# Kernel tuning notes

Measured on AMD Instinct MI355X. Metric: run time of the kernel, lower is better.

The kernel has to match this reference:

```python
import jax, jax.numpy as jnp
import numpy as np

B, C, H, W = 8, 192, 64, 64
RED = 8
CR = C // RED  # 24


def prelu(x, a):
    # a is a single shared slope (PyTorch nn.PReLU() default num_parameters=1)
    return jnp.where(x >= 0, x, a * x)


def conv1x1(x, w, b):
    # x: [B,C,H,W], w: [O,C], b: [O] -> [B,O,H,W]
    return jnp.einsum('bchw,oc->bohw', x, w) + b[None, :, None, None]


def setup_inputs() -> dict:
    key = jax.random.key(0)
    ks = jax.random.split(key, 7)
    scale1 = 1.0 / np.sqrt(C)
    return {
        'x': jax.random.normal(ks[0], (B, C, H, W), dtype=jnp.float32),
        'w1': jax.random.uniform(ks[1], (CR, C), jnp.float32, -scale1, scale1),
        'b1': jnp.zeros((CR,), jnp.float32),
        'a1': jnp.full((1,), 0.25, jnp.float32),
        'w2': jax.random.uniform(ks[2], (CR, C), jnp.float32, -scale1, scale1),
        'b2': jnp.zeros((CR,), jnp.float32),
        'a2': jnp.full((1,), 0.25, jnp.float32),
        'wa': jax.random.uniform(ks[3], (C, C), jnp.float32, -scale1, scale1),
        'ba': jnp.zeros((C,), jnp.float32),
        'aa': jnp.full((1,), 0.25, jnp.float32),
    }


def reference(x, w1, b1, a1, w2, b2, a2, wa, ba, aa):
    b, c, h, w = x.shape
    hw = h * w
    q = prelu(conv1x1(x, w1, b1), a1)          # [B,Cr,H,W]
    k = prelu(conv1x1(x, w2, b2), a2)          # [B,Cr,H,W]
    v = prelu(conv1x1(x, wa, ba), aa)          # [B,C,H,W]
    q = q.reshape(b, -1, hw).transpose(0, 2, 1)   # [B,HW,Cr]
    k = k.reshape(b, -1, hw)                      # [B,Cr,HW]
    score = jax.nn.softmax(jnp.einsum('bnc,bcm->bnm', q, k), axis=2)  # [B,HW,HW]
    v = v.reshape(b, c, hw).transpose(0, 2, 1)    # [B,HW,C]
    out = jnp.einsum('bnm,bmc->bnc', score, v)    # [B,HW,C]
    return out.transpose(0, 2, 1).reshape(b, c, h, w)
```

## Files before the change

kernel.cpp:

```cpp
#include <hip/hip_runtime.h>
#include <hip/hip_fp16.h>

#define HW 4096
#define NC 192
#define NB 8
#define DQK 32
#define LOG2E 1.4426950408889634f
#define THRL 11.541560327f

typedef _Float16 f16x8 __attribute__((ext_vector_type(8)));
typedef float f32x4 __attribute__((ext_vector_type(4)));
typedef unsigned int u32x4 __attribute__((ext_vector_type(4)));

#define BAR() do { asm volatile("s_waitcnt lgkmcnt(0)" ::: "memory"); \
                   __builtin_amdgcn_s_barrier();                      \
                   asm volatile("" ::: "memory"); } while (0)

static __device__ __forceinline__ unsigned int pkrtz(float a, float b) {
  auto h = __builtin_amdgcn_cvt_pkrtz(a, b);
  return __builtin_bit_cast(unsigned int, h);
}
static __device__ __forceinline__ unsigned short f2h_bits(float f) {
  _Float16 h = (_Float16)f;
  union { _Float16 h; unsigned short u; } cv; cv.h = h; return cv.u;
}

__global__ void wtrans_kernel(
    const float* __restrict__ w1, const float* __restrict__ b1, const float* __restrict__ a1,
    const float* __restrict__ w2, const float* __restrict__ b2, const float* __restrict__ a2,
    const float* __restrict__ wa, const float* __restrict__ ba, const float* __restrict__ aa,
    float* __restrict__ wt)
{
  const int c = blockIdx.x;
  const int o = threadIdx.x;
  if (o >= 240) return;
  float v;
  if (c < 192) {
    if (o < 24)      v = w1[o * 192 + c];
    else if (o < 48) v = w2[(o - 24) * 192 + c];
    else             v = wa[(o - 48) * 192 + c];
  } else if (c == 192) {
    v = (o < 24) ? b1[o] : (o < 48) ? b2[o - 24] : ba[o - 48];
  } else {
    v = (o < 24) ? a1[0] : (o < 48) ? a2[0] : aa[0];
  }
  wt[c * 240 + o] = v;
}

__global__ __launch_bounds__(256) void proj_kernel(
    const float* __restrict__ x, const float* __restrict__ wt,
    unsigned short* __restrict__ Qn, unsigned short* __restrict__ Kn,
    unsigned short* __restrict__ Vt)
{
  const int g   = blockIdx.y;
  const int tid = threadIdx.x;
  const int bp  = (blockIdx.x * 256 + tid) * 2;
  const int b   = bp >> 12;
  const int pos = bp & (HW - 1);

  const float* xb = x + (size_t)b * NC * HW + pos;
  float acc0[16], acc1[16];
  #pragma unroll
  for (int o = 0; o < 16; ++o) { acc0[o] = 0.f; acc1[o] = 0.f; }

  #pragma unroll 4
  for (int c = 0; c < 192; ++c) {
    float2 xv = *reinterpret_cast<const float2*>(xb + (size_t)c * HW);
    const float* wr = wt + c * 240 + g * 16;
    #pragma unroll
    for (int o = 0; o < 16; ++o) {
      float w = wr[o];
      acc0[o] = fmaf(w, xv.x, acc0[o]);
      acc1[o] = fmaf(w, xv.y, acc1[o]);
    }
  }

  const float* brow = wt + 192 * 240 + g * 16;
  const float* srow = wt + 193 * 240 + g * 16;
  unsigned short h0[16], h1[16];
  #pragma unroll
  for (int o = 0; o < 16; ++o) {
    float bias = brow[o], sm1 = srow[o] - 1.f;
    float v0 = acc0[o] + bias; v0 += fminf(v0, 0.f) * sm1;
    float v1 = acc1[o] + bias; v1 += fminf(v1, 0.f) * sm1;
    if (g * 16 + o < 24) { v0 *= LOG2E; v1 *= LOG2E; }
    h0[o] = f2h_bits(v0);
    h1[o] = f2h_bits(v1);
  }

  if (g >= 3) {
    const int vch0 = g * 16 - 48;
    unsigned int* vp = reinterpret_cast<unsigned int*>(
        Vt + ((size_t)b * NC + vch0) * HW + pos);
    #pragma unroll
    for (int o = 0; o < 16; ++o)
      vp[o * (HW / 2)] = (unsigned int)h0[o] | ((unsigned int)h1[o] << 16);
  } else {
    u32x4 lo0, hi0, lo1, hi1;
    #pragma unroll
    for (int j = 0; j < 4; ++j) {
      lo0[j] = (unsigned int)h0[2 * j] | ((unsigned int)h0[2 * j + 1] << 16);
      hi0[j] = (unsigned int)h0[8 + 2 * j] | ((unsigned int)h0[9 + 2 * j] << 16);
      lo1[j] = (unsigned int)h1[2 * j] | ((unsigned int)h1[2 * j + 1] << 16);
      hi1[j] = (unsigned int)h1[8 + 2 * j] | ((unsigned int)h1[9 + 2 * j] << 16);
    }
    const size_t bpos = (size_t)b * HW + pos;
    if (g == 0) {
      u32x4* q0 = reinterpret_cast<u32x4*>(Qn + bpos * DQK);
      q0[0] = lo0; q0[1] = hi0;
      u32x4* q1 = reinterpret_cast<u32x4*>(Qn + (bpos + 1) * DQK);
      q1[0] = lo1; q1[1] = hi1;
    } else if (g == 1) {
      *reinterpret_cast<u32x4*>(Qn + bpos * DQK + 16) = lo0;
      *reinterpret_cast<u32x4*>(Kn + bpos * DQK) = hi0;
      *reinterpret_cast<u32x4*>(Qn + (bpos + 1) * DQK + 16) = lo1;
      *reinterpret_cast<u32x4*>(Kn + (bpos + 1) * DQK) = hi1;
    } else {
      u32x4* k0 = reinterpret_cast<u32x4*>(Kn + bpos * DQK + 8);
      k0[0] = lo0; k0[1] = hi0;
      u32x4* k1 = reinterpret_cast<u32x4*>(Kn + (bpos + 1) * DQK + 8);
      k1[0] = lo1; k1[1] = hi1;
    }
  }
}

__global__ __launch_bounds__(512, 4) void flash_kernel(
    const unsigned short* __restrict__ Qn, const unsigned short* __restrict__ Kn,
    const unsigned short* __restrict__ Vt, float* __restrict__ out)
{
  const int b    = blockIdx.y;
  const int q0   = blockIdx.x * 64;
  const int tid  = threadIdx.x;
  const int w    = tid >> 6;
  const int half = w >> 2;
  const int wi   = w & 3;
  const int lane = tid & 63;
  const int lq   = lane & 15;
  const int lk   = lane >> 4;

  __shared__ u32x4 Pex[2][2][4][2][64];
  __shared__ float alphaL[2][2][4][16];
  __shared__ float mlL[2][2][64];

  const int mbase = half * (HW / 2);
  const int sigb  = 8 * (lq >> 2) + (lq & 3);

  f16x8 qfrag = *reinterpret_cast<const f16x8*>(
      Qn + ((size_t)b * HW + q0 + 16 * wi + lq) * DQK + 8 * lk);

  float m = -1e30f;
  f32x4 O[12], lacc;
  #pragma unroll
  for (int i = 0; i < 12; ++i) O[i] = (f32x4){0.f, 0.f, 0.f, 0.f};
  lacc = (f32x4){0.f, 0.f, 0.f, 0.f};

  const unsigned short* Kb = Kn + (size_t)b * HW * DQK + (size_t)sigb * DQK + 8 * lk;
  const unsigned short* Vw = Vt + (size_t)b * NC * HW + (size_t)(wi * 48 + lq) * HW + 8 * lk;

  f16x8 vones;
  #pragma unroll
  for (int i = 0; i < 8; ++i) vones[i] = (_Float16)1.0f;

  f16x8 Kf[4];

  auto qk_softmax = [&](int par) {
    f32x4 s[4];
    #pragma unroll
    for (int t = 0; t < 4; ++t)
      s[t] = __builtin_amdgcn_mfma_f32_16x16x32_f16(Kf[t], qfrag,
              (f32x4){0.f, 0.f, 0.f, 0.f}, 0, 0, 0);
    float pmax = s[0][0];
    #pragma unroll
    for (int t = 0; t < 4; ++t)
      #pragma unroll
      for (int r = 0; r < 4; ++r) pmax = fmaxf(pmax, s[t][r]);
    float alpha = 1.f;
    if (__any(pmax > m + THRL)) {
      pmax = fmaxf(pmax, __shfl_xor(pmax, 16));
      pmax = fmaxf(pmax, __shfl_xor(pmax, 32));
      float mn = fmaxf(m, pmax);
      alpha = exp2f(m - mn);
      m = mn;
    }
    float pv[4][4];
    #pragma unroll
    for (int t = 0; t < 4; ++t)
      #pragma unroll
      for (int r = 0; r < 4; ++r) pv[t][r] = exp2f(s[t][r] - m);
    u32x4 pa0, pa1;
    pa0[0] = pkrtz(pv[0][0], pv[0][1]); pa0[1] = pkrtz(pv[0][2], pv[0][3]);
    pa0[2] = pkrtz(pv[2][0], pv[2][1]); pa0[3] = pkrtz(pv[2][2], pv[2][3]);
    pa1[0] = pkrtz(pv[1][0], pv[1][1]); pa1[1] = pkrtz(pv[1][2], pv[1][3]);
    pa1[2] = pkrtz(pv[3][0], pv[3][1]); pa1[3] = pkrtz(pv[3][2], pv[3][3]);
    Pex[par][half][wi][0][lane] = pa0;
    Pex[par][half][wi][1][lane] = pa1;
    if (lane < 16) alphaL[par][half][wi][lane] = alpha;
  };

  #pragma unroll
  for (int t = 0; t < 4; ++t)
    Kf[t] = *reinterpret_cast<const f16x8*>(
        Kb + (size_t)(mbase + 32 * (t & 1) + 4 * (t >> 1)) * DQK);
  qk_softmax(0);
  BAR();

  const int NIT = HW / 2 / 64;
  for (int it = 0; it < NIT; ++it) {
    const int prt = it & 1;
    const bool notlast = (it + 1 < NIT);
    const int m0 = mbase + it * 64;
    const int mnext = m0 + 64;
    if (notlast) {
      #pragma unroll
      for (int t = 0; t < 4; ++t)
        Kf[t] = *reinterpret_cast<const f16x8*>(
            Kb + (size_t)(mnext + 32 * (t & 1) + 4 * (t >> 1)) * DQK);
    }
    #pragma unroll
    for (int tr = 0; tr < 4; ++tr) {
      f32x4 al = *reinterpret_cast<const f32x4*>(&alphaL[prt][half][tr][4 * lk]);
      int diff = (al[0] != 1.f) | (al[1] != 1.f) | (al[2] != 1.f) | (al[3] != 1.f);
      if (__any(diff)) {
        #pragma unroll
        for (int tc = 0; tc < 3; ++tc) {
          O[tr * 3 + tc][0] *= al[0]; O[tr * 3 + tc][1] *= al[1];
          O[tr * 3 + tc][2] *= al[2]; O[tr * 3 + tc][3] *= al[3];
        }
        if (tr == wi) {
          lacc[0] *= al[0]; lacc[1] *= al[1]; lacc[2] *= al[2]; lacc[3] *= al[3];
        }
      }
    }
    {
      f16x8 paf[4];
      #pragma unroll
      for (int tr = 0; tr < 4; ++tr)
        paf[tr] = __builtin_bit_cast(f16x8, Pex[prt][half][tr][0][lane]);
      f16x8 pw = __builtin_bit_cast(f16x8, Pex[prt][half][wi][0][lane]);
      lacc = __builtin_amdgcn_mfma_f32_16x16x32_f16(pw, vones, lacc, 0, 0, 0);
      #pragma unroll
      for (int tc = 0; tc < 3; ++tc) {
        f16x8 vb = *reinterpret_cast<const f16x8*>(
            Vw + (size_t)tc * 16 * HW + m0);
        #pragma unroll
        for (int tr = 0; tr < 4; ++tr)
          O[tr * 3 + tc] = __builtin_amdgcn_mfma_f32_16x16x32_f16(
              paf[tr], vb, O[tr * 3 + tc], 0, 0, 0);
      }
    }
    if (notlast) qk_softmax(prt ^ 1);
    {
      f16x8 paf[4];
      #pragma unroll
      for (int tr = 0; tr < 4; ++tr)
        paf[tr] = __builtin_bit_cast(f16x8, Pex[prt][half][tr][1][lane]);
      f16x8 pw = __builtin_bit_cast(f16x8, Pex[prt][half][wi][1][lane]);
      lacc = __builtin_amdgcn_mfma_f32_16x16x32_f16(pw, vones, lacc, 0, 0, 0);
      #pragma unroll
      for (int tc = 0; tc < 3; ++tc) {
        f16x8 vb = *reinterpret_cast<const f16x8*>(
            Vw + (size_t)tc * 16 * HW + m0 + 32);
        #pragma unroll
        for (int tr = 0; tr < 4; ++tr)
          O[tr * 3 + tc] = __builtin_amdgcn_mfma_f32_16x16x32_f16(
              paf[tr], vb, O[tr * 3 + tc], 0, 0, 0);
      }
    }
    BAR();
  }

  if (lane < 16) mlL[half][0][16 * wi + lane] = m;
  if (lq == 0) {
    #pragma unroll
    for (int r = 0; r < 4; ++r) mlL[half][1][16 * wi + 4 * lk + r] = lacc[r];
  }
  f32x4* Ost = reinterpret_cast<f32x4*>(&Pex[0][0][0][0][0]);
  if (half == 1) {
    #pragma unroll
    for (int i = 0; i < 8; ++i) Ost[(wi * 8 + i) * 64 + lane] = O[i];
  }
  BAR();
  f32x4 f0v[4], f1v[4];
  if (half == 0) {
    #pragma unroll
    for (int tr = 0; tr < 4; ++tr) {
      f32x4 m0v = *reinterpret_cast<const f32x4*>(&mlL[0][0][16 * tr + 4 * lk]);
      f32x4 l0v = *reinterpret_cast<const f32x4*>(&mlL[0][1][16 * tr + 4 * lk]);
      f32x4 m1v = *reinterpret_cast<const f32x4*>(&mlL[1][0][16 * tr + 4 * lk]);
      f32x4 l1v = *reinterpret_cast<const f32x4*>(&mlL[1][1][16 * tr + 4 * lk]);
      #pragma unroll
      for (int r = 0; r < 4; ++r) {
        float M  = fmaxf(m0v[r], m1v[r]);
        float s0 = exp2f(m0v[r] - M), s1 = exp2f(m1v[r] - M);
        float L  = s0 * l0v[r] + s1 * l1v[r];
        f0v[tr][r] = s0 / L; f1v[tr][r] = s1 / L;
      }
    }
    #pragma unroll
    for (int i = 0; i < 8; ++i) {
      const int tr = i / 3, tc = i - tr * 3;
      f32x4 o1 = Ost[(wi * 8 + i) * 64 + lane];
      f32x4 o;
      #pragma unroll
      for (int r = 0; r < 4; ++r) o[r] = O[i][r] * f0v[tr][r] + o1[r] * f1v[tr][r];
      *reinterpret_cast<f32x4*>(
          out + ((size_t)b * NC + wi * 48 + tc * 16 + lq) * HW + q0 + 16 * tr + 4 * lk) = o;
    }
  }
  BAR();
  if (half == 1) {
    #pragma unroll
    for (int i = 0; i < 4; ++i) Ost[(wi * 4 + i) * 64 + lane] = O[8 + i];
  }
  BAR();
  if (half == 0) {
    #pragma unroll
    for (int i = 8; i < 12; ++i) {
      const int tr = i / 3, tc = i - tr * 3;
      f32x4 o1 = Ost[(wi * 4 + (i - 8)) * 64 + lane];
      f32x4 o;
      #pragma unroll
      for (int r = 0; r < 4; ++r) o[r] = O[i][r] * f0v[tr][r] + o1[r] * f1v[tr][r];
      *reinterpret_cast<f32x4*>(
          out + ((size_t)b * NC + wi * 48 + tc * 16 + lq) * HW + q0 + 16 * tr + 4 * lk) = o;
    }
  }
}

extern "C" void kernel_launch(void* const* d_in, const int* in_sizes, int n_in,
                              void* d_out, int out_size, void* d_ws, size_t ws_size,
                              hipStream_t stream) {
  const float* x  = (const float*)d_in[0];
  const float* w1 = (const float*)d_in[1];
  const float* b1 = (const float*)d_in[2];
  const float* a1 = (const float*)d_in[3];
  const float* w2 = (const float*)d_in[4];
  const float* b2 = (const float*)d_in[5];
  const float* a2 = (const float*)d_in[6];
  const float* wa = (const float*)d_in[7];
  const float* ba = (const float*)d_in[8];
  const float* aa = (const float*)d_in[9];
  float* out = (float*)d_out;

  unsigned short* Qn = (unsigned short*)d_ws;
  unsigned short* Kn = Qn + (size_t)NB * HW * DQK;
  unsigned short* Vt = Kn + (size_t)NB * HW * DQK;
  float* wt = out + (out_size - 49152);

  (void)hipMemsetAsync(Qn, 0, (size_t)NB * HW * DQK * 2 * sizeof(unsigned short), stream);

  wtrans_kernel<<<dim3(194), 256, 0, stream>>>(w1, b1, a1, w2, b2, a2, wa, ba, aa, wt);

  dim3 pgrid(HW * NB / 512, 15);
  proj_kernel<<<pgrid, 256, 0, stream>>>(x, wt, Qn, Kn, Vt);

  dim3 fgrid(HW / 64, NB);
  flash_kernel<<<fgrid, 512, 0, stream>>>(Qn, Kn, Vt, out);
}
```

Before: 184.0 us.

## Restructure projection to 48 channels per thread and hoist V loads with MFMA priority

```diff
diff --git a/kernel.cpp b/kernel.cpp
--- a/kernel.cpp
+++ b/kernel.cpp
@@ -53,74 +53,57 @@
     unsigned short* __restrict__ Vt)
 {
   const int g   = blockIdx.y;
-  const int tid = threadIdx.x;
-  const int bp  = (blockIdx.x * 256 + tid) * 2;
+  const int bp  = blockIdx.x * 256 + threadIdx.x;
   const int b   = bp >> 12;
   const int pos = bp & (HW - 1);
+  const int ob  = 48 * g;
 
   const float* xb = x + (size_t)b * NC * HW + pos;
-  float acc0[16], acc1[16];
-  #pragma unroll
-  for (int o = 0; o < 16; ++o) { acc0[o] = 0.f; acc1[o] = 0.f; }
-
-  #pragma unroll 4
+  float acc[48];
+  #pragma unroll
+  for (int o = 0; o < 48; ++o) acc[o] = 0.f;
+
+  #pragma unroll 2
   for (int c = 0; c < 192; ++c) {
-    float2 xv = *reinterpret_cast<const float2*>(xb + (size_t)c * HW);
-    const float* wr = wt + c * 240 + g * 16;
-    #pragma unroll
-    for (int o = 0; o < 16; ++o) {
-      float w = wr[o];
-      acc0[o] = fmaf(w, xv.x, acc0[o]);
-      acc1[o] = fmaf(w, xv.y, acc1[o]);
-    }
-  }
-
-  const float* brow = wt + 192 * 240 + g * 16;
-  const float* srow = wt + 193 * 240 + g * 16;
-  unsigned short h0[16], h1[16];
-  #pragma unroll
-  for (int o = 0; o < 16; ++o) {
+    float xv = xb[(size_t)c * HW];
+    const float* wr = wt + c * 240 + ob;
+    #pragma unroll
+    for (int o = 0; o < 48; ++o) acc[o] = fmaf(wr[o], xv, acc[o]);
+  }
+
+  const float* brow = wt + 192 * 240 + ob;
+  const float* srow = wt + 193 * 240 + ob;
+  unsigned short h[48];
+  #pragma unroll
+  for (int o = 0; o < 48; ++o) {
     float bias = brow[o], sm1 = srow[o] - 1.f;
-    float v0 = acc0[o] + bias; v0 += fminf(v0, 0.f) * sm1;
-    float v1 = acc1[o] + bias; v1 += fminf(v1, 0.f) * sm1;
-    if (g * 16 + o < 24) { v0 *= LOG2E; v1 *= LOG2E; }
-    h0[o] = f2h_bits(v0);
-    h1[o] = f2h_bits(v1);
-  }
-
-  if (g >= 3) {
-    const int vch0 = g * 16 - 48;
-    unsigned int* vp = reinterpret_cast<unsigned int*>(
-        Vt + ((size_t)b * NC + vch0) * HW + pos);
-    #pragma unroll
-    for (int o = 0; o < 16; ++o)
-      vp[o * (HW / 2)] = (unsigned int)h0[o] | ((unsigned int)h1[o] << 16);
+    float v = acc[o] + bias; v += fminf(v, 0.f) * sm1;
+    if (g == 0 && o < 24) v *= LOG2E;
+    h[o] = f2h_bits(v);
+  }
+
+  if (g == 0) {
+    const size_t bpos = (size_t)bp;
+    u32x4 u;
+    #pragma unroll
+    for (int j = 0; j < 3; ++j) {
+      #pragma unroll
+      for (int i = 0; i < 4; ++i)
+        u[i] = (unsigned int)h[8 * j + 2 * i] | ((unsigned int)h[8 * j + 2 * i + 1] << 16);
+      *reinterpret_cast<u32x4*>(Qn + bpos * DQK + 8 * j) = u;
+    }
+    #pragma unroll
+    for (int j = 0; j < 3; ++j) {
+      #pragma unroll
+      for (int i = 0; i < 4; ++i)
+        u[i] = (unsigned int)h[24 + 8 * j + 2 * i] | ((unsigned int)h[25 + 8 * j + 2 * i] << 16);
+      *reinterpret_cast<u32x4*>(Kn + bpos * DQK + 8 * j) = u;
+    }
   } else {
-    u32x4 lo0, hi0, lo1, hi1;
-    #pragma unroll
-    for (int j = 0; j < 4; ++j) {
-      lo0[j] = (unsigned int)h0[2 * j] | ((unsigned int)h0[2 * j + 1] << 16);
-      hi0[j] = (unsigned int)h0[8 + 2 * j] | ((unsigned int)h0[9 + 2 * j] << 16);
-      lo1[j] = (unsigned int)h1[2 * j] | ((unsigned int)h1[2 * j + 1] << 16);
-      hi1[j] = (unsigned int)h1[8 + 2 * j] | ((unsigned int)h1[9 + 2 * j] << 16);
-    }
-    const size_t bpos = (size_t)b * HW + pos;
-    if (g == 0) {
-      u32x4* q0 = reinterpret_cast<u32x4*>(Qn + bpos * DQK);
-      q0[0] = lo0; q0[1] = hi0;
-      u32x4* q1 = reinterpret_cast<u32x4*>(Qn + (bpos + 1) * DQK);
-      q1[0] = lo1; q1[1] = hi1;
-    } else if (g == 1) {
-      *reinterpret_cast<u32x4*>(Qn + bpos * DQK + 16) = lo0;
-      *reinterpret_cast<u32x4*>(Kn + bpos * DQK) = hi0;
-      *reinterpret_cast<u32x4*>(Qn + (bpos + 1) * DQK + 16) = lo1;
-      *reinterpret_cast<u32x4*>(Kn + (bpos + 1) * DQK) = hi1;
-    } else {
-      u32x4* k0 = reinterpret_cast<u32x4*>(Kn + bpos * DQK + 8);
-      k0[0] = lo0; k0[1] = hi0;
-      u32x4* k1 = reinterpret_cast<u32x4*>(Kn + (bpos + 1) * DQK + 8);
-      k1[0] = lo1; k1[1] = hi1;
-    }
+    const int vch0 = 48 * (g - 1);
+    #pragma unroll
+    for (int o = 0; o < 48; ++o)
+      Vt[((size_t)b * NC + vch0 + o) * HW + pos] = h[o];
   }
 }
 
@@ -128,8 +111,8 @@
     const unsigned short* __restrict__ Qn, const unsigned short* __restrict__ Kn,
     const unsigned short* __restrict__ Vt, float* __restrict__ out)
 {
-  const int b    = blockIdx.y;
-  const int q0   = blockIdx.x * 64;
+  const int b    = blockIdx.x & 7;
+  const int q0   = (blockIdx.x >> 3) * 64;
   const int tid  = threadIdx.x;
   const int w    = tid >> 6;
   const int half = w >> 2;
@@ -210,6 +193,10 @@
     const bool notlast = (it + 1 < NIT);
     const int m0 = mbase + it * 64;
     const int mnext = m0 + 64;
+    f16x8 vb0[3];
+    #pragma unroll
+    for (int tc = 0; tc < 3; ++tc)
+      vb0[tc] = *reinterpret_cast<const f16x8*>(Vw + (size_t)tc * 16 * HW + m0);
     if (notlast) {
       #pragma unroll
       for (int t = 0; t < 4; ++t)
@@ -237,17 +224,20 @@
       for (int tr = 0; tr < 4; ++tr)
         paf[tr] = __builtin_bit_cast(f16x8, Pex[prt][half][tr][0][lane]);
       f16x8 pw = __builtin_bit_cast(f16x8, Pex[prt][half][wi][0][lane]);
+      __builtin_amdgcn_s_setprio(1);
       lacc = __builtin_amdgcn_mfma_f32_16x16x32_f16(pw, vones, lacc, 0, 0, 0);
       #pragma unroll
-      for (int tc = 0; tc < 3; ++tc) {
-        f16x8 vb = *reinterpret_cast<const f16x8*>(
-            Vw + (size_t)tc * 16 * HW + m0);
+      for (int tc = 0; tc < 3; ++tc)
         #pragma unroll
         for (int tr = 0; tr < 4; ++tr)
           O[tr * 3 + tc] = __builtin_amdgcn_mfma_f32_16x16x32_f16(
-              paf[tr], vb, O[tr * 3 + tc], 0, 0, 0);
-      }
-    }
+              paf[tr], vb0[tc], O[tr * 3 + tc], 0, 0, 0);
+      __builtin_amdgcn_s_setprio(0);
+    }
+    f16x8 vb1[3];
+    #pragma unroll
+    for (int tc = 0; tc < 3; ++tc)
+      vb1[tc] = *reinterpret_cast<const f16x8*>(Vw + (size_t)tc * 16 * HW + m0 + 32);
     if (notlast) qk_softmax(prt ^ 1);
     {
       f16x8 paf[4];
@@ -255,16 +245,15 @@
       for (int tr = 0; tr < 4; ++tr)
         paf[tr] = __builtin_bit_cast(f16x8, Pex[prt][half][tr][1][lane]);
       f16x8 pw = __builtin_bit_cast(f16x8, Pex[prt][half][wi][1][lane]);
+      __builtin_amdgcn_s_setprio(1);
       lacc = __builtin_amdgcn_mfma_f32_16x16x32_f16(pw, vones, lacc, 0, 0, 0);
       #pragma unroll
-      for (int tc = 0; tc < 3; ++tc) {
-        f16x8 vb = *reinterpret_cast<const f16x8*>(
-            Vw + (size_t)tc * 16 * HW + m0 + 32);
+      for (int tc = 0; tc < 3; ++tc)
         #pragma unroll
         for (int tr = 0; tr < 4; ++tr)
           O[tr * 3 + tc] = __builtin_amdgcn_mfma_f32_16x16x32_f16(
-              paf[tr], vb, O[tr * 3 + tc], 0, 0, 0);
-      }
+              paf[tr], vb1[tc], O[tr * 3 + tc], 0, 0, 0);
+      __builtin_amdgcn_s_setprio(0);
     }
     BAR();
   }
@@ -351,9 +340,8 @@
 
   wtrans_kernel<<<dim3(194), 256, 0, stream>>>(w1, b1, a1, w2, b2, a2, wa, ba, aa, wt);
 
-  dim3 pgrid(HW * NB / 512, 15);
+  dim3 pgrid(HW * NB / 256, 5);
   proj_kernel<<<pgrid, 256, 0, stream>>>(x, wt, Qn, Kn, Vt);
 
-  dim3 fgrid(HW / 64, NB);
-  flash_kernel<<<fgrid, 512, 0, stream>>>(Qn, Kn, Vt, out);
-}
+  flash_kernel<<<dim3(512), 512, 0, stream>>>(Qn, Kn, Vt, out);
+}
```

After: 242.4 us. 1.32x slower.
